# Performance work log

Measured on AMD Instinct MI355X. Metric: run time of the kernel, lower is better.

The kernel has to match this reference:

```python
import jax, jax.numpy as jnp
import numpy as np

N = 50000      # nodes
E = 800000     # edges (avg degree 16)
IN = 128       # in_dim
OUT = 128      # out_dim
K = 4          # Chebyshev order
NEIG = 64      # num_eigs
H = 128        # eigval_hidden_dim
BN_EPS = 1e-5


def setup_inputs() -> dict:
    key = jax.random.key(0)
    ks = jax.random.split(key, 12)
    feature = jax.random.normal(ks[0], (N, IN), jnp.float32)
    # linear over concat of (K Chebyshev blocks + 1 spectral block) = (K+1)*IN
    lin_w = jax.random.normal(ks[1], ((K + 1) * IN, OUT), jnp.float32) / np.sqrt((K + 1) * IN)
    lin_b = jnp.zeros((OUT,), jnp.float32)
    # eigval_filter MLP: 1 -> H -> H -> 1 (ReLU between)
    ew0 = jax.random.normal(ks[2], (1, H), jnp.float32)
    eb0 = jnp.zeros((H,), jnp.float32)
    ew1 = jax.random.normal(ks[3], (H, H), jnp.float32) / np.sqrt(H)
    eb1 = jnp.zeros((H,), jnp.float32)
    ew2 = jax.random.normal(ks[4], (H, 1), jnp.float32) / np.sqrt(H)
    eb2 = jnp.zeros((1,), jnp.float32)
    bn_gamma = jnp.ones((OUT,), jnp.float32)
    bn_beta = jnp.zeros((OUT,), jnp.float32)
    lambda_max = jnp.ones((1,), jnp.float32)
    # cached (detached) spectral data for the graph
    evecs = jax.random.normal(ks[5], (N, NEIG), jnp.float32)
    evals = jax.random.uniform(ks[6], (NEIG,), jnp.float32)
    edge_src = jax.random.randint(ks[7], (E,), 0, N, jnp.int32).astype(jnp.int64)
    edge_dst = jax.random.randint(ks[8], (E,), 0, N, jnp.int32).astype(jnp.int64)
    return dict(feature=feature, lin_w=lin_w, lin_b=lin_b, ew0=ew0, eb0=eb0,
                ew1=ew1, eb1=eb1, ew2=ew2, eb2=eb2, bn_gamma=bn_gamma,
                bn_beta=bn_beta, lambda_max=lambda_max, evecs=evecs,
                evals=evals, edge_src=edge_src, edge_dst=edge_dst)


def reference(feature, lin_w, lin_b, ew0, eb0, ew1, eb1, ew2, eb2,
              bn_gamma, bn_beta, lambda_max, evecs, evals, edge_src, edge_dst):
    src = edge_src.astype(jnp.int32)
    dst = edge_dst.astype(jnp.int32)
    # in-degrees (messages arrive at dst) and D^-1/2, clamped at 1
    deg = jax.ops.segment_sum(jnp.ones((E,), jnp.float32), dst, num_segments=N)
    d_sqrt = jnp.clip(deg, 1.0, None) ** -0.5  # [N]
    d_sqrt = d_sqrt[:, None]                   # [N,1]

    def unn_laplacian(x):
        m = (x * d_sqrt)[src]                              # [E,IN]
        agg = jax.ops.segment_sum(m, dst, num_segments=N)  # [N,IN]
        return agg * d_sqrt

    re_norm = 2.0 / lambda_max  # broadcast scalar (per-node in dgl, constant here)

    X0 = feature
    blocks = [X0]
    h = unn_laplacian(X0)
    X1 = -re_norm * h + X0 * (re_norm - 1.0)
    blocks.append(X1)
    for _ in range(2, K):
        h = unn_laplacian(X1)
        Xi = -2.0 * re_norm * h + X1 * 2.0 * (re_norm - 1.0) - X0
        blocks.append(Xi)
        X1, X0 = Xi, X1

    # spectral filtering: evecs^T f, scale by MLP(evals), project back
    z = jax.nn.relu(evals[:, None] @ ew0 + eb0)   # [NEIG,H]
    z = jax.nn.relu(z @ ew1 + eb1)                # [NEIG,H]
    ef = z @ ew2 + eb2                            # [NEIG,1]
    hs = jnp.einsum('ne,nf->ef', evecs, feature)  # [NEIG,IN]
    hs = ef * hs
    hs = jnp.einsum('ne,ef->nf', evecs, hs)       # [N,IN]
    blocks.append(hs)

    Xt = jnp.concatenate(blocks, axis=1)          # [N,(K+1)*IN]
    out = Xt @ lin_w + lin_b                      # [N,OUT]

    # BatchNorm1d (training-mode batch statistics, biased variance)
    mu = jnp.mean(out, axis=0)
    var = jnp.mean((out - mu) ** 2, axis=0)
    out = (out - mu) * jax.lax.rsqrt(var + BN_EPS) * bn_gamma + bn_beta
    out = jax.nn.relu(out)
    # dropout p=0.0 -> identity; residual disabled
    return out
```

## Files before the change

### kernel.cpp

```cpp
#include <hip/hip_runtime.h>

#define N_NODES 50000
#define N_EDGES 800000
#define IN_F    128
#define OUT_F   128
#define NEIG    64
#define HDIM    128
#define BN_EPSF 1e-5f
#define XB_ROWS 50048
#define XB_COLS 640
#define SCAN_BLK 49
#define HSP_BLOCKS 521
#define HSP_NODES 96
#define RED_CHUNK 33
#define N_CHK 32
#define N_RNG 4
#define RANKB (N_RNG * N_CHK)
#define CHUNK_E (N_EDGES / N_CHK)

typedef __attribute__((ext_vector_type(8))) short short8;
typedef __attribute__((ext_vector_type(4))) float floatx4;

#define OFF_XB      0
#define OFF_X1F     (XB_ROWS * XB_COLS / 2)
#define OFF_X2F     (OFF_X1F + N_NODES * IN_F)
#define OFF_DEGC    OFF_X2F
#define OFF_RSC     (OFF_X2F + N_CHK * N_NODES)
#define OFF_WT      (OFF_X2F + N_NODES * IN_F)
#define OFF_DSQRT   (OFF_WT + 40960)
#define OFF_HS      (OFF_DSQRT + N_NODES)
#define OFF_EF      (OFF_HS + NEIG * OUT_F)
#define OFF_COLSUM  (OFF_EF + NEIG)
#define OFF_COLSQ   (OFF_COLSUM + OUT_F)
#define OFF_DEG     (OFF_COLSQ + OUT_F)
#define OFF_ROWSTART (OFF_DEG + 8 * N_NODES)
#define OFF_CSR     (OFF_ROWSTART + N_NODES + 1)
#define OFF_BSUM    (OFF_CSR + N_EDGES)
#define OFF_RANK    (OFF_BSUM + 64)

static __device__ inline unsigned short f2bf(float f) {
    union { float f; unsigned int u; } v; v.f = f;
    unsigned int r = (v.u + 0x7FFFu + ((v.u >> 16) & 1u)) >> 16;
    return (unsigned short)r;
}
static __device__ inline float bf2f(unsigned int u16) {
    union { unsigned int u; float f; } v; v.u = u16 << 16;
    return v.f;
}

__global__ __launch_bounds__(256) void k_prep(const float* __restrict__ feat,
                                              const float* __restrict__ W,
                                              unsigned short* __restrict__ Xb,
                                              unsigned short* __restrict__ Wt,
                                              float* __restrict__ small) {
    int b = blockIdx.x;
    if (b < 3125) {
        int t = b * 256 + threadIdx.x;
        int n = t >> 4, c8 = (t & 15) * 8;
        float4 a = *(const float4*)&feat[n * IN_F + c8];
        float4 bb = *(const float4*)&feat[n * IN_F + c8 + 4];
        ushort4 o0, o1;
        o0.x = f2bf(a.x); o0.y = f2bf(a.y); o0.z = f2bf(a.z); o0.w = f2bf(a.w);
        o1.x = f2bf(bb.x); o1.y = f2bf(bb.y); o1.z = f2bf(bb.z); o1.w = f2bf(bb.w);
        *(ushort4*)&Xb[(size_t)n * XB_COLS + c8]     = o0;
        *(ushort4*)&Xb[(size_t)n * XB_COLS + c8 + 4] = o1;
    } else if (b < 3445) {
        int t = (b - 3125) * 256 + threadIdx.x;
        int k = t >> 7, n = t & 127;
        Wt[n * 640 + k] = f2bf(W[k * 128 + n]);
    } else {
        int i = (b - 3445) * 256 + threadIdx.x;
        if (i < NEIG * OUT_F + NEIG + 2 * OUT_F) small[i] = 0.0f;
    }
}

struct HsSm  { float sEv[32 * NEIG]; float sFt[32 * IN_F]; };
struct MlpSm { float z0[2][HDIM]; float red[2][HDIM]; };
union StageSm {
    HsSm hs;
    MlpSm mlp;
    unsigned int cnt[6250];
};

__global__ __launch_bounds__(256) void k_stage2(const float* __restrict__ evecs,
                                                const float* __restrict__ feat,
                                                float* __restrict__ partials,
                                                const float* __restrict__ evals,
                                                const float* __restrict__ ew0,
                                                const float* __restrict__ eb0,
                                                const float* __restrict__ ew1,
                                                const float* __restrict__ eb1,
                                                const float* __restrict__ ew2,
                                                const float* __restrict__ eb2,
                                                float* __restrict__ ef,
                                                int* __restrict__ degC,
                                                const int* __restrict__ dst,
                                                int* __restrict__ rank) {
    __shared__ __align__(16) StageSm sm;
    int b = blockIdx.x;
    int t = threadIdx.x;
    if (b < HSP_BLOCKS) {
        float* sEv = sm.hs.sEv;
        float* sFt = sm.hs.sFt;
        int e0 = (t >> 5) * 8;
        int f0 = (t & 31) * 4;
        float acc[8][4];
#pragma unroll
        for (int r = 0; r < 8; ++r)
#pragma unroll
            for (int c = 0; c < 4; ++c) acc[r][c] = 0.0f;

        int n0 = b * HSP_NODES;
        for (int ch = 0; ch < HSP_NODES; ch += 32) {
            int base = n0 + ch;
            {
                int r = t >> 3, c = (t & 7) * 8;
                int n = base + r;
                float4 a, bb;
                if (n < N_NODES) {
                    a = *(const float4*)&evecs[(size_t)n * NEIG + c];
                    bb = *(const float4*)&evecs[(size_t)n * NEIG + c + 4];
                } else {
                    a = make_float4(0, 0, 0, 0); bb = a;
                }
                *(float4*)&sEv[r * NEIG + c] = a;
                *(float4*)&sEv[r * NEIG + c + 4] = bb;
            }
            {
                int r = t >> 3, c = (t & 7) * 16;
                int n = base + r;
#pragma unroll
                for (int q = 0; q < 4; ++q) {
                    float4 v = (n < N_NODES) ? *(const float4*)&feat[(size_t)n * IN_F + c + q * 4]
                                             : make_float4(0, 0, 0, 0);
                    *(float4*)&sFt[r * IN_F + c + q * 4] = v;
                }
            }
            __syncthreads();
#pragma unroll 2
            for (int i = 0; i < 32; ++i) {
                float4 ev0 = *(float4*)&sEv[i * NEIG + e0];
                float4 ev1 = *(float4*)&sEv[i * NEIG + e0 + 4];
                float4 fv  = *(float4*)&sFt[i * IN_F + f0];
                float evv[8] = {ev0.x, ev0.y, ev0.z, ev0.w, ev1.x, ev1.y, ev1.z, ev1.w};
#pragma unroll
                for (int r = 0; r < 8; ++r) {
                    acc[r][0] += evv[r] * fv.x;
                    acc[r][1] += evv[r] * fv.y;
                    acc[r][2] += evv[r] * fv.z;
                    acc[r][3] += evv[r] * fv.w;
                }
            }
            __syncthreads();
        }
        float* p = &partials[(size_t)b * (NEIG * IN_F)];
#pragma unroll
        for (int r = 0; r < 8; ++r)
            *(float4*)&p[(e0 + r) * IN_F + f0] = make_float4(acc[r][0], acc[r][1], acc[r][2], acc[r][3]);
    } else if (b < HSP_BLOCKS + 32) {
        int sub = t >> 7, j = t & 127;
        int i = (b - HSP_BLOCKS) * 2 + sub;
        float ev = evals[i];
        sm.mlp.z0[sub][j] = fmaxf(0.0f, ev * ew0[j] + eb0[j]);
        __syncthreads();
        float s0 = 0.f, s1 = 0.f, s2 = 0.f, s3 = 0.f;
        for (int h = 0; h < HDIM; h += 4) {
            s0 += sm.mlp.z0[sub][h]     * ew1[(h) * HDIM + j];
            s1 += sm.mlp.z0[sub][h + 1] * ew1[(h + 1) * HDIM + j];
            s2 += sm.mlp.z0[sub][h + 2] * ew1[(h + 2) * HDIM + j];
            s3 += sm.mlp.z0[sub][h + 3] * ew1[(h + 3) * HDIM + j];
        }
        float z1 = fmaxf(0.0f, eb1[j] + s0 + s1 + s2 + s3);
        sm.mlp.red[sub][j] = z1 * ew2[j];
        __syncthreads();
        for (int off = 64; off > 0; off >>= 1) {
            if (j < off) sm.mlp.red[sub][j] += sm.mlp.red[sub][j + off];
            __syncthreads();
        }
        if (j == 0) ef[i] = sm.mlp.red[sub][0] + eb2[0];
    } else {
        unsigned int* cnt = sm.cnt;
        int rb = b - (HSP_BLOCKS + 32);
        int g = rb >> 5, c = rb & (N_CHK - 1);
        for (int k = t; k < 6250; k += 256) cnt[k] = 0;
        __syncthreads();
        int nlo = g * 12500;
        int ebase = c * CHUNK_E;
        for (int off0 = 0; off0 < CHUNK_E; off0 += 1024) {
            int d0[4];
#pragma unroll
            for (int k = 0; k < 4; ++k) {
                int o = off0 + k * 256 + t;
                d0[k] = (o < CHUNK_E) ? dst[ebase + o] : -1;
            }
#pragma unroll
            for (int k = 0; k < 4; ++k) {
                int o = off0 + k * 256 + t;
                int l = d0[k] - nlo;
                if ((unsigned)l < 12500u) {
                    unsigned sh = (l & 1) * 16;
                    unsigned old = atomicAdd(&cnt[l >> 1], 1u << sh);
                    rank[ebase + o] = ((old >> sh) & 0xFFFF) | (c << 24);
                }
            }
        }
        __syncthreads();
        for (int k = t; k < 6250; k += 256) {
            unsigned v = cnt[k];
            int n0 = nlo + k * 2;
            degC[(size_t)c * N_NODES + n0]     = (int)(v & 0xFFFF);
            degC[(size_t)c * N_NODES + n0 + 1] = (int)(v >> 16);
        }
    }
}

__global__ __launch_bounds__(1024) void k_stage3(int* __restrict__ degC,
                                                 int* __restrict__ row_start,
                                                 int* __restrict__ bsum,
                                                 const float* __restrict__ partials,
                                                 float* __restrict__ hs_small) {
    int b = blockIdx.x;
    int t = threadIdx.x;
    if (b < SCAN_BLK) {
        __shared__ int sd[1024];
        int i = b * 1024 + t;
        int total = 0;
        if (i < N_NODES) {
#pragma unroll 8
            for (int cc = 0; cc < N_CHK; ++cc)
                total += degC[(size_t)cc * N_NODES + i];
        }
        sd[t] = total;
        __syncthreads();
        for (int off = 1; off < 1024; off <<= 1) {
            int v = (t >= off) ? sd[t - off] : 0;
            __syncthreads();
            sd[t] += v;
            __syncthreads();
        }
        if (i < N_NODES) {
            row_start[i] = sd[t] - total;
            int p = degC[i];
            for (int cc = 1; cc < N_CHK; ++cc) {
                int v = degC[(size_t)cc * N_NODES + i];
                degC[(size_t)cc * N_NODES + i] = p;
                p += v;
            }
            degC[i] = p;
        }
        if (t == 1023) bsum[b] = sd[1023];
    } else {
        int b2 = b - SCAN_BLK;
        int grp = b2 & 7;
        int chunk = b2 >> 3;
        int idx = grp * 1024 + t;
        int j0 = chunk * RED_CHUNK;
        int j1 = min(j0 + RED_CHUNK, HSP_BLOCKS);
        float s = 0.0f;
        for (int j = j0; j < j1; ++j) s += partials[(size_t)j * (NEIG * IN_F) + idx];
        atomicAdd(&hs_small[idx], s);
    }
}

__global__ __launch_bounds__(1024) void k_scan3(const int* __restrict__ degC,
                                                int* __restrict__ row_start,
                                                const int* __restrict__ bsum,
                                                float* __restrict__ dsq,
                                                int* __restrict__ rsC) {
    __shared__ int sOff;
    int t = threadIdx.x;
    if (t < 64) {
        int orig = (t < SCAN_BLK) ? bsum[t] : 0;
        int v = orig;
        for (int off = 1; off < 64; off <<= 1) {
            int u = __shfl_up(v, off);
            if (t >= off) v += u;
        }
        if (t == blockIdx.x) sOff = v - orig;
    }
    __syncthreads();
    int i = blockIdx.x * 1024 + t;
    if (i < N_NODES) {
        int r = row_start[i] + sOff;
        row_start[i] = r;
        rsC[i] = r;
        for (int cc = 1; cc < N_CHK; ++cc)
            rsC[(size_t)cc * N_NODES + i] = r + degC[(size_t)cc * N_NODES + i];
        dsq[i] = rsqrtf((float)max(degC[i], 1));
    }
    if (i == 0) row_start[N_NODES] = N_EDGES;
}

__global__ __launch_bounds__(256) void k_stage6(const int* __restrict__ src,
                                                const int* __restrict__ dst,
                                                const int* __restrict__ rank,
                                                const int* __restrict__ rsC,
                                                int* __restrict__ csr_src,
                                                unsigned short* __restrict__ Xb,
                                                const float* __restrict__ evecs,
                                                const float* __restrict__ hs_small,
                                                const float* __restrict__ ef) {
    int b = blockIdx.x;
    int t = threadIdx.x;
    if (b < 3125) {
        int e = b * 256 + t;
        if (e < N_EDGES) {
            int rv = rank[e];
            int c = rv >> 24;
            csr_src[rsC[(size_t)c * N_NODES + dst[e]] + (rv & 0xFFFFFF)] = src[e];
        }
    } else {
        __shared__ float sShs[NEIG * HDIM];
        __shared__ float sEv[32 * NEIG];
        int n0 = (b - 3125) * 32;
        {
            float efv = ef[t >> 2];
            int pbase = t * 32;
#pragma unroll
            for (int q = 0; q < 8; ++q) {
                float4 v = *(const float4*)&hs_small[pbase + q * 4];
                v.x *= efv; v.y *= efv; v.z *= efv; v.w *= efv;
                *(float4*)&sShs[pbase + q * 4] = v;
            }
        }
        {
            int r = t >> 3, c = (t & 7) * 8;
            int n = n0 + r;
            float4 a, bb;
            if (n < N_NODES) {
                a = *(const float4*)&evecs[(size_t)n * NEIG + c];
                bb = *(const float4*)&evecs[(size_t)n * NEIG + c + 4];
            } else {
                a = make_float4(0, 0, 0, 0); bb = a;
            }
            *(float4*)&sEv[r * NEIG + c] = a;
            *(float4*)&sEv[r * NEIG + c + 4] = bb;
        }
        __syncthreads();
        int nb = (t >> 5) * 4;
        int f0 = (t & 31) * 4;
        float acc[4][4];
#pragma unroll
        for (int q = 0; q < 4; ++q)
#pragma unroll
            for (int c = 0; c < 4; ++c) acc[q][c] = 0.0f;
        for (int e = 0; e < NEIG; ++e) {
            float4 sv = *(float4*)&sShs[e * HDIM + f0];
#pragma unroll
            for (int q = 0; q < 4; ++q) {
                float evv = sEv[(nb + q) * NEIG + e];
                acc[q][0] += evv * sv.x;
                acc[q][1] += evv * sv.y;
                acc[q][2] += evv * sv.z;
                acc[q][3] += evv * sv.w;
            }
        }
#pragma unroll
        for (int q = 0; q < 4; ++q) {
            int n = n0 + nb + q;
            if (n < N_NODES) {
                ushort4 o;
                o.x = f2bf(acc[q][0]); o.y = f2bf(acc[q][1]);
                o.z = f2bf(acc[q][2]); o.w = f2bf(acc[q][3]);
                *(ushort4*)&Xb[(size_t)n * XB_COLS + 4 * IN_F + f0] = o;
            }
        }
    }
}

__global__ __launch_bounds__(256) void k_gather(const int* __restrict__ row_start,
                                                const int* __restrict__ csr_src,
                                                const float* __restrict__ dsq,
                                                const unsigned short* __restrict__ srcb,
                                                const unsigned short* __restrict__ prevb,
                                                const unsigned short* __restrict__ ppb,
                                                unsigned short* __restrict__ outb,
                                                const float* __restrict__ lm, int first) {
    int n = (blockIdx.x * 256 + threadIdx.x) >> 6;
    int lane = threadIdx.x & 63;
    if (n >= N_NODES) return;
    float rn = 2.0f / lm[0];
    float ax = 0.0f, ay = 0.0f;
    int beg = row_start[n], end = row_start[n + 1];
    int i = beg;
    for (; i + 16 <= end; i += 16) {
        int s[16]; float c[16]; unsigned int p[16];
#pragma unroll
        for (int j = 0; j < 16; ++j) s[j] = __builtin_amdgcn_readfirstlane(csr_src[i + j]);
#pragma unroll
        for (int j = 0; j < 16; ++j) c[j] = dsq[s[j]];
#pragma unroll
        for (int j = 0; j < 16; ++j)
            p[j] = *(const unsigned int*)&srcb[(size_t)s[j] * XB_COLS + lane * 2];
#pragma unroll
        for (int j = 0; j < 16; ++j) {
            ax += c[j] * bf2f(p[j] & 0xffffu);
            ay += c[j] * bf2f(p[j] >> 16);
        }
    }
    for (; i + 8 <= end; i += 8) {
        int s[8]; float c[8]; unsigned int p[8];
#pragma unroll
        for (int j = 0; j < 8; ++j) s[j] = __builtin_amdgcn_readfirstlane(csr_src[i + j]);
#pragma unroll
        for (int j = 0; j < 8; ++j) c[j] = dsq[s[j]];
#pragma unroll
        for (int j = 0; j < 8; ++j)
            p[j] = *(const unsigned int*)&srcb[(size_t)s[j] * XB_COLS + lane * 2];
#pragma unroll
        for (int j = 0; j < 8; ++j) {
            ax += c[j] * bf2f(p[j] & 0xffffu);
            ay += c[j] * bf2f(p[j] >> 16);
        }
    }
    for (; i + 4 <= end; i += 4) {
        int s[4]; float c[4]; unsigned int p[4];
#pragma unroll
        for (int j = 0; j < 4; ++j) s[j] = __builtin_amdgcn_readfirstlane(csr_src[i + j]);
#pragma unroll
        for (int j = 0; j < 4; ++j) c[j] = dsq[s[j]];
#pragma unroll
        for (int j = 0; j < 4; ++j)
            p[j] = *(const unsigned int*)&srcb[(size_t)s[j] * XB_COLS + lane * 2];
#pragma unroll
        for (int j = 0; j < 4; ++j) {
            ax += c[j] * bf2f(p[j] & 0xffffu);
            ay += c[j] * bf2f(p[j] >> 16);
        }
    }
    for (; i < end; ++i) {
        int s = __builtin_amdgcn_readfirstlane(csr_src[i]);
        float sc = dsq[s];
        unsigned int pv = *(const unsigned int*)&srcb[(size_t)s * XB_COLS + lane * 2];
        ax += sc * bf2f(pv & 0xffffu);
        ay += sc * bf2f(pv >> 16);
    }
    float ds = dsq[n];
    float a = (first ? -rn : -2.0f * rn) * ds;
    float b = first ? (rn - 1.0f) : 2.0f * (rn - 1.0f);
    unsigned int pu = *(const unsigned int*)&prevb[(size_t)n * XB_COLS + lane * 2];
    float rx = a * ax + b * bf2f(pu & 0xffffu);
    float ry = a * ay + b * bf2f(pu >> 16);
    if (ppb) {
        unsigned int qu = *(const unsigned int*)&ppb[(size_t)n * XB_COLS + lane * 2];
        rx -= bf2f(qu & 0xffffu);
        ry -= bf2f(qu >> 16);
    }
    unsigned int packed = (unsigned int)f2bf(rx) | ((unsigned int)f2bf(ry) << 16);
    *(unsigned int*)&outb[(size_t)n * XB_COLS + lane * 2] = packed;
}

__global__ __launch_bounds__(256) void k_gemm(const unsigned short* __restrict__ Xb,
                                              const unsigned short* __restrict__ Wt,
                                              const float* __restrict__ bias,
                                              float* __restrict__ out,
                                              float* __restrict__ colsum,
                                              float* __restrict__ colsq) {
    __shared__ unsigned short sA[128 * 32];
    __shared__ unsigned short sB[128 * 32];
    __shared__ float cs[4][OUT_F];
    __shared__ float cq[4][OUT_F];
    int tid = threadIdx.x;
    int wave = tid >> 6, lane = tid & 63;
    int quad = lane >> 4, m16 = lane & 15;
    int row0 = blockIdx.x * 128;

    floatx4 acc[2][8];
#pragma unroll
    for (int mt = 0; mt < 2; ++mt)
#pragma unroll
        for (int nt = 0; nt < 8; ++nt) acc[mt][nt] = (floatx4)(0.0f);

    int r  = tid >> 2;
    int c8 = (tid & 3) * 8;
    int gr0 = min(row0 + r, N_NODES - 1);
    int gr1 = min(row0 + r + 64, N_NODES - 1);

    for (int k0 = 0; k0 < 640; k0 += 32) {
        *(uint4*)&sA[r * 32 + c8]        = *(const uint4*)&Xb[(size_t)gr0 * XB_COLS + k0 + c8];
        *(uint4*)&sA[(r + 64) * 32 + c8] = *(const uint4*)&Xb[(size_t)gr1 * XB_COLS + k0 + c8];
        *(uint4*)&sB[r * 32 + c8]        = *(const uint4*)&Wt[r * 640 + k0 + c8];
        *(uint4*)&sB[(r + 64) * 32 + c8] = *(const uint4*)&Wt[(r + 64) * 640 + k0 + c8];
        __syncthreads();
        short8 a0 = *(short8*)&sA[(wave * 32 + m16) * 32 + quad * 8];
        short8 a1 = *(short8*)&sA[(wave * 32 + 16 + m16) * 32 + quad * 8];
#pragma unroll
        for (int nt = 0; nt < 8; ++nt) {
            short8 b = *(short8*)&sB[(nt * 16 + m16) * 32 + quad * 8];
            acc[0][nt] = __builtin_amdgcn_mfma_f32_16x16x32_bf16(a0, b, acc[0][nt], 0, 0, 0);
            acc[1][nt] = __builtin_amdgcn_mfma_f32_16x16x32_bf16(a1, b, acc[1][nt], 0, 0, 0);
        }
        __syncthreads();
    }
#pragma unroll
    for (int nt = 0; nt < 8; ++nt) {
        int col = nt * 16 + m16;
        float bb = bias[col];
        float sv = 0.0f, sq = 0.0f;
#pragma unroll
        for (int mt = 0; mt < 2; ++mt) {
            int rbase = row0 + wave * 32 + mt * 16 + quad * 4;
#pragma unroll
            for (int reg = 0; reg < 4; ++reg) {
                int row = rbase + reg;
                if (row < N_NODES) {
                    float w = acc[mt][nt][reg] + bb;
                    out[(size_t)row * OUT_F + col] = w;
                    sv += w;
                    sq += w * w;
                }
            }
        }
        sv += __shfl_down(sv, 32); sq += __shfl_down(sq, 32);
        sv += __shfl_down(sv, 16); sq += __shfl_down(sq, 16);
        if (lane < 16) { cs[wave][col] = sv; cq[wave][col] = sq; }
    }
    __syncthreads();
    if (tid < OUT_F) {
        float s = cs[0][tid] + cs[1][tid] + cs[2][tid] + cs[3][tid];
        float q = cq[0][tid] + cq[1][tid] + cq[2][tid] + cq[3][tid];
        atomicAdd(&colsum[tid], s);
        atomicAdd(&colsq[tid], q);
    }
}

__global__ void k_bn_apply(float* __restrict__ out, const float* __restrict__ colsum,
                           const float* __restrict__ colsq, const float* __restrict__ gamma,
                           const float* __restrict__ beta) {
    int t = blockIdx.x * 256 + threadIdx.x;
    int n = t >> 5, c = t & 31;
    float4 v = *(float4*)&out[n * OUT_F + c * 4];
    float4 s = *(const float4*)&colsum[c * 4];
    float4 q = *(const float4*)&colsq[c * 4];
    float4 g = *(const float4*)&gamma[c * 4];
    float4 b = *(const float4*)&beta[c * 4];
    const float invN = 1.0f / (float)N_NODES;
    float mux = s.x * invN, muy = s.y * invN, muz = s.z * invN, muw = s.w * invN;
    float ix = rsqrtf(q.x * invN - mux * mux + BN_EPSF);
    float iy = rsqrtf(q.y * invN - muy * muy + BN_EPSF);
    float iz = rsqrtf(q.z * invN - muz * muz + BN_EPSF);
    float iw = rsqrtf(q.w * invN - muw * muw + BN_EPSF);
    v.x = fmaxf(0.0f, (v.x - mux) * ix * g.x + b.x);
    v.y = fmaxf(0.0f, (v.y - muy) * iy * g.y + b.y);
    v.z = fmaxf(0.0f, (v.z - muz) * iz * g.z + b.z);
    v.w = fmaxf(0.0f, (v.w - muw) * iw * g.w + b.w);
    *(float4*)&out[n * OUT_F + c * 4] = v;
}

extern "C" void kernel_launch(void* const* d_in, const int* in_sizes, int n_in,
                              void* d_out, int out_size, void* d_ws, size_t ws_size,
                              hipStream_t stream) {
    const float* feature    = (const float*)d_in[0];
    const float* lin_w      = (const float*)d_in[1];
    const float* lin_b      = (const float*)d_in[2];
    const float* ew0        = (const float*)d_in[3];
    const float* eb0        = (const float*)d_in[4];
    const float* ew1        = (const float*)d_in[5];
    const float* eb1        = (const float*)d_in[6];
    const float* ew2        = (const float*)d_in[7];
    const float* eb2        = (const float*)d_in[8];
    const float* bn_gamma   = (const float*)d_in[9];
    const float* bn_beta    = (const float*)d_in[10];
    const float* lambda_max = (const float*)d_in[11];
    const float* evecs      = (const float*)d_in[12];
    const float* evals      = (const float*)d_in[13];
    const int*   edge_src   = (const int*)d_in[14];
    const int*   edge_dst   = (const int*)d_in[15];

    float* out = (float*)d_out;
    float* ws  = (float*)d_ws;
    unsigned short* Xb = (unsigned short*)(ws + OFF_XB);
    unsigned short* Wt = (unsigned short*)(ws + OFF_WT);
    float* dsq      = ws + OFF_DSQRT;
    float* hs_small = ws + OFF_HS;
    float* ef       = ws + OFF_EF;
    float* colsum   = ws + OFF_COLSUM;
    float* colsq    = ws + OFF_COLSQ;
    int*   degC     = (int*)(ws + OFF_DEGC);
    int*   rsC      = (int*)(ws + OFF_RSC);
    int*   row_start= (int*)(ws + OFF_ROWSTART);
    int*   csr_src  = (int*)(ws + OFF_CSR);
    int*   bsum     = (int*)(ws + OFF_BSUM);
    int*   rank     = (int*)(ws + OFF_RANK);
    float* partials = ws + OFF_X1F;

    k_prep<<<3479, 256, 0, stream>>>(feature, lin_w, Xb, Wt, hs_small);

    k_stage2<<<HSP_BLOCKS + 32 + RANKB, 256, 0, stream>>>(evecs, feature, partials,
                                                          evals, ew0, eb0, ew1, eb1, ew2, eb2,
                                                          ef, degC, edge_dst, rank);

    k_stage3<<<SCAN_BLK + 128, 1024, 0, stream>>>(degC, row_start, bsum, partials, hs_small);
    k_scan3<<<SCAN_BLK, 1024, 0, stream>>>(degC, row_start, bsum, dsq, rsC);

    k_stage6<<<3125 + 1563, 256, 0, stream>>>(edge_src, edge_dst, rank, rsC, csr_src,
                                              Xb, evecs, hs_small, ef);

    const int GBLK = (N_NODES * 64 + 255) / 256;
    k_gather<<<GBLK, 256, 0, stream>>>(row_start, csr_src, dsq,
                                       Xb + 0, Xb + 0, (const unsigned short*)nullptr,
                                       Xb + IN_F, lambda_max, 1);
    k_gather<<<GBLK, 256, 0, stream>>>(row_start, csr_src, dsq,
                                       Xb + IN_F, Xb + IN_F, Xb + 0,
                                       Xb + 2 * IN_F, lambda_max, 0);
    k_gather<<<GBLK, 256, 0, stream>>>(row_start, csr_src, dsq,
                                       Xb + 2 * IN_F, Xb + 2 * IN_F, Xb + IN_F,
                                       Xb + 3 * IN_F, lambda_max, 0);

    k_gemm<<<(N_NODES + 127) / 128, 256, 0, stream>>>(Xb, Wt, lin_b, out, colsum, colsq);
    k_bn_apply<<<(N_NODES * 32) / 256, 256, 0, stream>>>(out, colsum, colsq, bn_gamma, bn_beta);
}
```

Measured before the change: 329.4 us.

## Fold prep into stage2 and replace separate scan kernel with cross-block lookback

Moves the bf16 conversion, weight transpose and zeroing work into the stage2 kernel as extra block ranges. Replaces the second scan kernel with an in-kernel cross-block offset exchange, where each scan block publishes its total with a flag and spins on all predecessors. This removes two kernel launches and their gaps. In exchange it relies on all scan blocks being co-resident and on the flag array being zeroed in the earlier kernel.

```diff
diff --git a/kernel.cpp b/kernel.cpp
--- a/kernel.cpp
+++ b/kernel.cpp
@@ -18,6 +18,12 @@
 #define RANKB (N_RNG * N_CHK)
 #define CHUNK_E (N_EDGES / N_CHK)
 
+#define S2_MLP   (HSP_BLOCKS + 32)
+#define S2_RANK  (S2_MLP + RANKB)
+#define S2_FEAT  (S2_RANK + 3125)
+#define S2_WT    (S2_FEAT + 320)
+#define S2_END   (S2_WT + 35)
+
 typedef __attribute__((ext_vector_type(8))) short short8;
 typedef __attribute__((ext_vector_type(4))) float floatx4;
 
@@ -32,8 +38,8 @@
 #define OFF_EF      (OFF_HS + NEIG * OUT_F)
 #define OFF_COLSUM  (OFF_EF + NEIG)
 #define OFF_COLSQ   (OFF_COLSUM + OUT_F)
-#define OFF_DEG     (OFF_COLSQ + OUT_F)
-#define OFF_ROWSTART (OFF_DEG + 8 * N_NODES)
+#define OFF_PUB     (OFF_COLSQ + OUT_F)
+#define OFF_ROWSTART (OFF_PUB + 8 * N_NODES)
 #define OFF_CSR     (OFF_ROWSTART + N_NODES + 1)
 #define OFF_BSUM    (OFF_CSR + N_EDGES)
 #define OFF_RANK    (OFF_BSUM + 64)
@@ -46,32 +52,6 @@
 static __device__ inline float bf2f(unsigned int u16) {
     union { unsigned int u; float f; } v; v.u = u16 << 16;
     return v.f;
-}
-
-__global__ __launch_bounds__(256) void k_prep(const float* __restrict__ feat,
-                                              const float* __restrict__ W,
-                                              unsigned short* __restrict__ Xb,
-                                              unsigned short* __restrict__ Wt,
-                                              float* __restrict__ small) {
-    int b = blockIdx.x;
-    if (b < 3125) {
-        int t = b * 256 + threadIdx.x;
-        int n = t >> 4, c8 = (t & 15) * 8;
-        float4 a = *(const float4*)&feat[n * IN_F + c8];
-        float4 bb = *(const float4*)&feat[n * IN_F + c8 + 4];
-        ushort4 o0, o1;
-        o0.x = f2bf(a.x); o0.y = f2bf(a.y); o0.z = f2bf(a.z); o0.w = f2bf(a.w);
-        o1.x = f2bf(bb.x); o1.y = f2bf(bb.y); o1.z = f2bf(bb.z); o1.w = f2bf(bb.w);
-        *(ushort4*)&Xb[(size_t)n * XB_COLS + c8]     = o0;
-        *(ushort4*)&Xb[(size_t)n * XB_COLS + c8 + 4] = o1;
-    } else if (b < 3445) {
-        int t = (b - 3125) * 256 + threadIdx.x;
-        int k = t >> 7, n = t & 127;
-        Wt[n * 640 + k] = f2bf(W[k * 128 + n]);
-    } else {
-        int i = (b - 3445) * 256 + threadIdx.x;
-        if (i < NEIG * OUT_F + NEIG + 2 * OUT_F) small[i] = 0.0f;
-    }
 }
 
 struct HsSm  { float sEv[32 * NEIG]; float sFt[32 * IN_F]; };
@@ -95,7 +75,12 @@
                                                 float* __restrict__ ef,
                                                 int* __restrict__ degC,
                                                 const int* __restrict__ dst,
-                                                int* __restrict__ rank) {
+                                                int* __restrict__ rank,
+                                                const float* __restrict__ W,
+                                                unsigned short* __restrict__ Xb,
+                                                unsigned short* __restrict__ Wt,
+                                                float* __restrict__ small,
+                                                int* __restrict__ pubz) {
     __shared__ __align__(16) StageSm sm;
     int b = blockIdx.x;
     int t = threadIdx.x;
@@ -157,7 +142,7 @@
 #pragma unroll
         for (int r = 0; r < 8; ++r)
             *(float4*)&p[(e0 + r) * IN_F + f0] = make_float4(acc[r][0], acc[r][1], acc[r][2], acc[r][3]);
-    } else if (b < HSP_BLOCKS + 32) {
+    } else if (b < S2_MLP) {
         int sub = t >> 7, j = t & 127;
         int i = (b - HSP_BLOCKS) * 2 + sub;
         float ev = evals[i];
@@ -178,9 +163,9 @@
             __syncthreads();
         }
         if (j == 0) ef[i] = sm.mlp.red[sub][0] + eb2[0];
-    } else {
+    } else if (b < S2_RANK) {
         unsigned int* cnt = sm.cnt;
-        int rb = b - (HSP_BLOCKS + 32);
+        int rb = b - S2_MLP;
         int g = rb >> 5, c = rb & (N_CHK - 1);
         for (int k = t; k < 6250; k += 256) cnt[k] = 0;
         __syncthreads();
@@ -211,18 +196,40 @@
             degC[(size_t)c * N_NODES + n0]     = (int)(v & 0xFFFF);
             degC[(size_t)c * N_NODES + n0 + 1] = (int)(v >> 16);
         }
+    } else if (b < S2_FEAT) {
+        int tt = (b - S2_RANK) * 256 + t;
+        int n = tt >> 4, c8 = (tt & 15) * 8;
+        float4 a = *(const float4*)&feat[n * IN_F + c8];
+        float4 bb = *(const float4*)&feat[n * IN_F + c8 + 4];
+        ushort4 o0, o1;
+        o0.x = f2bf(a.x); o0.y = f2bf(a.y); o0.z = f2bf(a.z); o0.w = f2bf(a.w);
+        o1.x = f2bf(bb.x); o1.y = f2bf(bb.y); o1.z = f2bf(bb.z); o1.w = f2bf(bb.w);
+        *(ushort4*)&Xb[(size_t)n * XB_COLS + c8]     = o0;
+        *(ushort4*)&Xb[(size_t)n * XB_COLS + c8 + 4] = o1;
+    } else if (b < S2_WT) {
+        int tt = (b - S2_FEAT) * 256 + t;
+        int k = tt >> 7, n = tt & 127;
+        Wt[n * 640 + k] = f2bf(W[k * 128 + n]);
+    } else {
+        int i = (b - S2_WT) * 256 + t;
+        const int HSZ = NEIG * OUT_F;
+        if (i < HSZ || (i >= HSZ + NEIG && i < HSZ + NEIG + 2 * OUT_F)) small[i] = 0.0f;
+        if (i < 128) pubz[i] = 0;
     }
 }
 
 __global__ __launch_bounds__(1024) void k_stage3(int* __restrict__ degC,
                                                  int* __restrict__ row_start,
-                                                 int* __restrict__ bsum,
+                                                 unsigned long long* __restrict__ pub,
                                                  const float* __restrict__ partials,
-                                                 float* __restrict__ hs_small) {
+                                                 float* __restrict__ hs_small,
+                                                 float* __restrict__ dsq,
+                                                 int* __restrict__ rsC) {
     int b = blockIdx.x;
     int t = threadIdx.x;
     if (b < SCAN_BLK) {
         __shared__ int sd[1024];
+        __shared__ int sOff;
         int i = b * 1024 + t;
         int total = 0;
         if (i < N_NODES) {
@@ -238,17 +245,36 @@
             sd[t] += v;
             __syncthreads();
         }
+        if (t == 0) {
+            unsigned long long pv = (1ull << 32) | (unsigned long long)(unsigned)sd[1023];
+            __hip_atomic_store(&pub[b], pv, __ATOMIC_RELEASE, __HIP_MEMORY_SCOPE_AGENT);
+        }
+        if (t < 64) {
+            int tot = 0;
+            if (t < SCAN_BLK) {
+                unsigned long long v;
+                do {
+                    v = __hip_atomic_load(&pub[t], __ATOMIC_ACQUIRE, __HIP_MEMORY_SCOPE_AGENT);
+                } while (!(v >> 32));
+                tot = (int)(v & 0xffffffffu);
+            }
+            int contrib = (t < b) ? tot : 0;
+            for (int off = 32; off > 0; off >>= 1) contrib += __shfl_down(contrib, off);
+            if (t == 0) sOff = contrib;
+        }
+        __syncthreads();
         if (i < N_NODES) {
-            row_start[i] = sd[t] - total;
-            int p = degC[i];
-            for (int cc = 1; cc < N_CHK; ++cc) {
+            int r = sd[t] - total + sOff;
+            row_start[i] = r;
+            int p = r;
+            for (int cc = 0; cc < N_CHK; ++cc) {
                 int v = degC[(size_t)cc * N_NODES + i];
-                degC[(size_t)cc * N_NODES + i] = p;
+                rsC[(size_t)cc * N_NODES + i] = p;
                 p += v;
             }
-            degC[i] = p;
-        }
-        if (t == 1023) bsum[b] = sd[1023];
+            dsq[i] = rsqrtf((float)max(total, 1));
+        }
+        if (i == N_NODES - 1) row_start[N_NODES] = N_EDGES;
     } else {
         int b2 = b - SCAN_BLK;
         int grp = b2 & 7;
@@ -260,35 +286,6 @@
         for (int j = j0; j < j1; ++j) s += partials[(size_t)j * (NEIG * IN_F) + idx];
         atomicAdd(&hs_small[idx], s);
     }
-}
-
-__global__ __launch_bounds__(1024) void k_scan3(const int* __restrict__ degC,
-                                                int* __restrict__ row_start,
-                                                const int* __restrict__ bsum,
-                                                float* __restrict__ dsq,
-                                                int* __restrict__ rsC) {
-    __shared__ int sOff;
-    int t = threadIdx.x;
-    if (t < 64) {
-        int orig = (t < SCAN_BLK) ? bsum[t] : 0;
-        int v = orig;
-        for (int off = 1; off < 64; off <<= 1) {
-            int u = __shfl_up(v, off);
-            if (t >= off) v += u;
-        }
-        if (t == blockIdx.x) sOff = v - orig;
-    }
-    __syncthreads();
-    int i = blockIdx.x * 1024 + t;
-    if (i < N_NODES) {
-        int r = row_start[i] + sOff;
-        row_start[i] = r;
-        rsC[i] = r;
-        for (int cc = 1; cc < N_CHK; ++cc)
-            rsC[(size_t)cc * N_NODES + i] = r + degC[(size_t)cc * N_NODES + i];
-        dsq[i] = rsqrtf((float)max(degC[i], 1));
-    }
-    if (i == 0) row_start[N_NODES] = N_EDGES;
 }
 
 __global__ __launch_bounds__(256) void k_stage6(const int* __restrict__ src,
@@ -580,18 +577,18 @@
     int*   rsC      = (int*)(ws + OFF_RSC);
     int*   row_start= (int*)(ws + OFF_ROWSTART);
     int*   csr_src  = (int*)(ws + OFF_CSR);
-    int*   bsum     = (int*)(ws + OFF_BSUM);
     int*   rank     = (int*)(ws + OFF_RANK);
+    int*   pubz     = (int*)(ws + OFF_PUB);
+    unsigned long long* pub = (unsigned long long*)(ws + OFF_PUB);
     float* partials = ws + OFF_X1F;
 
-    k_prep<<<3479, 256, 0, stream>>>(feature, lin_w, Xb, Wt, hs_small);
-
-    k_stage2<<<HSP_BLOCKS + 32 + RANKB, 256, 0, stream>>>(evecs, feature, partials,
-                                                          evals, ew0, eb0, ew1, eb1, ew2, eb2,
-                                                          ef, degC, edge_dst, rank);
-
-    k_stage3<<<SCAN_BLK + 128, 1024, 0, stream>>>(degC, row_start, bsum, partials, hs_small);
-    k_scan3<<<SCAN_BLK, 1024, 0, stream>>>(degC, row_start, bsum, dsq, rsC);
+    k_stage2<<<S2_END, 256, 0, stream>>>(evecs, feature, partials,
+                                         evals, ew0, eb0, ew1, eb1, ew2, eb2,
+                                         ef, degC, edge_dst, rank,
+                                         lin_w, Xb, Wt, hs_small, pubz);
+
+    k_stage3<<<SCAN_BLK + 128, 1024, 0, stream>>>(degC, row_start, pub, partials,
+                                                  hs_small, dsq, rsC);
 
     k_stage6<<<3125 + 1563, 256, 0, stream>>>(edge_src, edge_dst, rank, rsC, csr_src,
                                               Xb, evecs, hs_small, ef);
```

Measured after the change: 330.6 us. Within noise of the previous version (+0.4%).
